# Kernel tuning notes

Hardware: AMD Instinct MI355X
Metric: run time of the kernel (lower is better)

The kernel has to match this reference:

```python
import jax, jax.numpy as jnp
import numpy as np

B, S, D, H = 2, 2048, 768, 12
DK = D // H
NEG = -1000000000.0


def setup_inputs() -> dict:
    key = jax.random.key(0)
    ks = jax.random.split(key, 12)
    inp = {
        "query": jax.random.normal(ks[0], (B, S, D), jnp.float32),
        "key": jax.random.normal(ks[1], (B, S, D), jnp.float32),
        "value": jax.random.normal(ks[2], (B, S, D), jnp.float32),
        "mask": jax.random.randint(ks[3], (B, 1, 1, S), 0, 2, jnp.int32),
    }
    sc = 1.0 / np.sqrt(D)
    inp["Wq"] = jax.random.normal(ks[4], (D, D), jnp.float32) * sc
    inp["bq"] = jnp.zeros((D,), jnp.float32)
    inp["Wk"] = jax.random.normal(ks[5], (D, D), jnp.float32) * sc
    inp["bk"] = jnp.zeros((D,), jnp.float32)
    inp["Wv"] = jax.random.normal(ks[6], (D, D), jnp.float32) * sc
    inp["bv"] = jnp.zeros((D,), jnp.float32)
    inp["Wo"] = jax.random.normal(ks[7], (D, D), jnp.float32) * sc
    inp["bo"] = jnp.zeros((D,), jnp.float32)
    return inp


def reference(query, key, value, mask, Wq, bq, Wk, bk, Wv, bv, Wo, bo):
    b = query.shape[0]
    # QKV projections -> [B, H, S, DK]
    def proj(x, W, bias):
        y = jnp.einsum('bsd,de->bse', x, W.T) + bias
        return y.reshape(b, -1, H, DK).transpose(0, 2, 1, 3)
    q = proj(query, Wq, bq)
    k = proj(key, Wk, bk)
    v = proj(value, Wv, bv)
    # scores: [B, H, S, S]
    scores = jnp.einsum('bhqd,bhkd->bhqk', q, k) / jnp.sqrt(jnp.float32(DK))
    scores = jnp.where(mask == 0, jnp.float32(NEG), scores)
    p = jax.nn.softmax(scores, axis=-1)
    x = jnp.einsum('bhqk,bhkd->bhqd', p, v)  # [B, H, S, DK]
    x = x.transpose(0, 2, 1, 3).reshape(b, -1, H * DK)
    return jnp.einsum('bsd,de->bse', x, Wo.T) + bo
```

## Files before the change

### kernel.cpp

```cpp
#include <hip/hip_runtime.h>

typedef unsigned short u16;
typedef __attribute__((ext_vector_type(8))) __bf16 bf16x8;
typedef __attribute__((ext_vector_type(8))) short s16x8;
typedef __attribute__((ext_vector_type(8))) unsigned short u16x8;
typedef __attribute__((ext_vector_type(4))) float f32x4;
typedef __attribute__((ext_vector_type(4))) unsigned short u16x4;
typedef __attribute__((ext_vector_type(4))) float fl4;
typedef __attribute__((ext_vector_type(4))) int i32x4;

#define MFMA(a, b, c) __builtin_amdgcn_mfma_f32_16x16x32_bf16((a), (b), (c), 0, 0, 0)
#define QSC 0.18033688011112042f

__device__ __forceinline__ u16 f2bf(float f) {
  __bf16 h = (__bf16)f;
  return __builtin_bit_cast(unsigned short, h);
}

__device__ __forceinline__ float bf2f(u16 u) {
  union { unsigned u; float f; } v; v.u = ((unsigned)u) << 16;
  return v.f;
}

__device__ __forceinline__ void gll16(const u16* g, u16* l) {
  typedef __attribute__((address_space(1))) unsigned int gu32;
  typedef __attribute__((address_space(3))) unsigned int lu32;
  __builtin_amdgcn_global_load_lds((gu32*)g, (lu32*)l, 16, 0, 0);
}


__global__ __launch_bounds__(256) void k_convert_w(
    const float* __restrict__ Wq, const float* __restrict__ Wk,
    const float* __restrict__ Wv, const float* __restrict__ Wo,
    u16* __restrict__ wqkv, u16* __restrict__ wob) {
  const int n = 3072 * 192;
  for (int i = blockIdx.x * 256 + threadIdx.x; i < n; i += gridDim.x * 256) {
    int row = i / 192;
    int col = (i - row * 192) * 4;
    const float* src; u16* dst; float sc = 1.0f;
    if (row < 768)       { src = Wq + row * 768;          dst = wqkv + row * 768; sc = QSC; }
    else if (row < 1536) { src = Wk + (row - 768) * 768;  dst = wqkv + row * 768; }
    else if (row < 2304) { src = Wv + (row - 1536) * 768; dst = wqkv + row * 768; }
    else                 { src = Wo + (row - 2304) * 768; dst = wob + (row - 2304) * 768; }
    fl4 f = *(const fl4*)(src + col);
    u16x4 o;
    o[0] = f2bf(f[0] * sc); o[1] = f2bf(f[1] * sc);
    o[2] = f2bf(f[2] * sc); o[3] = f2bf(f[3] * sc);
    *(u16x4*)(dst + col) = o;
  }
}


__global__ __launch_bounds__(256) void k_gemm_qkv(
    const float* __restrict__ xq, const float* __restrict__ xk,
    const float* __restrict__ xv, const u16* __restrict__ wqkv,
    const float* __restrict__ bq, const float* __restrict__ bk_,
    const float* __restrict__ bv_,
    u16* __restrict__ Qb, u16* __restrict__ Kb, u16* __restrict__ Vtb) {
  __shared__ __align__(16) u16 Abuf[2][128 * 32];
  __shared__ __align__(16) u16 Bbuf[2][128 * 32];
  const int tid = threadIdx.x;
  const int row0 = blockIdx.x * 128, col0 = blockIdx.y * 128;
  const int seg = col0 / 768;
  const float* A32 = (seg == 0) ? xq : ((seg == 1) ? xk : xv);
  const int w = tid >> 6, lane = tid & 63, lr = lane & 15, kg = lane >> 4;
  const int wr = (w >> 1) * 64, wc = (w & 1) * 64;

  const int c0 = tid, c1 = tid + 256;
  const int r0c = c0 >> 2, g0 = (c0 & 3) ^ ((r0c >> 1) & 3);
  const int r1c = c1 >> 2, g1 = (c1 & 3) ^ ((r1c >> 1) & 3);
  const float* aS0 = A32 + (size_t)(row0 + r0c) * 768 + g0 * 8;
  const float* aS1 = A32 + (size_t)(row0 + r1c) * 768 + g1 * 8;
  const u16* bS0 = wqkv + (size_t)(col0 + r0c) * 768 + g0 * 8;
  const u16* bS1 = wqkv + (size_t)(col0 + r1c) * 768 + g1 * 8;

  f32x4 acc[4][4];
  f32x4 zero = {0.f, 0.f, 0.f, 0.f};
#pragma unroll
  for (int i = 0; i < 4; i++)
#pragma unroll
    for (int j = 0; j < 4; j++) acc[i][j] = zero;

  int aoff[4], boff[4];
#pragma unroll
  for (int mi = 0; mi < 4; mi++) {
    int r = wr + mi * 16 + lr;
    aoff[mi] = r * 32 + (kg ^ ((r >> 1) & 3)) * 8;
  }
#pragma unroll
  for (int ni = 0; ni < 4; ni++) {
    int r = wc + ni * 16 + lr;
    boff[ni] = r * 32 + (kg ^ ((r >> 1) & 3)) * 8;
  }

  fl4 ar[4];
#define LOADA(kt) { ar[0] = *(const fl4*)(aS0 + (kt) * 32);       \
                    ar[1] = *(const fl4*)(aS0 + (kt) * 32 + 4);   \
                    ar[2] = *(const fl4*)(aS1 + (kt) * 32);       \
                    ar[3] = *(const fl4*)(aS1 + (kt) * 32 + 4); }
#define WRITEA(buf) { u16x8 t0, t1;                               \
    t0[0]=f2bf(ar[0][0]); t0[1]=f2bf(ar[0][1]); t0[2]=f2bf(ar[0][2]); t0[3]=f2bf(ar[0][3]); \
    t0[4]=f2bf(ar[1][0]); t0[5]=f2bf(ar[1][1]); t0[6]=f2bf(ar[1][2]); t0[7]=f2bf(ar[1][3]); \
    t1[0]=f2bf(ar[2][0]); t1[1]=f2bf(ar[2][1]); t1[2]=f2bf(ar[2][2]); t1[3]=f2bf(ar[2][3]); \
    t1[4]=f2bf(ar[3][0]); t1[5]=f2bf(ar[3][1]); t1[6]=f2bf(ar[3][2]); t1[7]=f2bf(ar[3][3]); \
    *(u16x8*)((buf) + c0 * 8) = t0; *(u16x8*)((buf) + c1 * 8) = t1; }
#define STAGEB(kt, buf) { gll16(bS0 + (kt) * 32, (buf) + c0 * 8); \
                          gll16(bS1 + (kt) * 32, (buf) + c1 * 8); }

  LOADA(0);
  STAGEB(0, Bbuf[0]);
  WRITEA(Abuf[0]);
  __syncthreads();

  for (int kt = 0; kt < 24; kt++) {
    const int cur = kt & 1;
    if (kt < 23) { LOADA(kt + 1); STAGEB(kt + 1, Bbuf[cur ^ 1]); }
    bf16x8 af[4], bfr[4];
#pragma unroll
    for (int mi = 0; mi < 4; mi++) af[mi] = *(const bf16x8*)(Abuf[cur] + aoff[mi]);
#pragma unroll
    for (int ni = 0; ni < 4; ni++) bfr[ni] = *(const bf16x8*)(Bbuf[cur] + boff[ni]);
#pragma unroll
    for (int mi = 0; mi < 4; mi++)
#pragma unroll
      for (int ni = 0; ni < 4; ni++)
        acc[mi][ni] = MFMA(af[mi], bfr[ni], acc[mi][ni]);
    __syncthreads();
    if (kt < 23) {
      WRITEA(Abuf[cur ^ 1]);
      __syncthreads();
    }
  }
#undef LOADA
#undef WRITEA
#undef STAGEB

  const float* bias = (seg == 0) ? bq : ((seg == 1) ? bk_ : bv_);
  const float bsc = (seg == 0) ? QSC : 1.0f;
  const int ncol0 = col0 - seg * 768;
#pragma unroll
  for (int ni = 0; ni < 4; ni++) {
    const int n = ncol0 + wc + ni * 16 + lr;
    const float bval = bias[n] * bsc;
    const int hh = n >> 6, dk = n & 63;
#pragma unroll
    for (int mi = 0; mi < 4; mi++)
#pragma unroll
      for (int j = 0; j < 4; j++) {
        const int m = row0 + wr + mi * 16 + kg * 4 + j;
        const int bb = m >> 11, ss = m & 2047;
        const u16 val = f2bf(acc[mi][ni][j] + bval);
        if (seg == 0)
          Qb[((size_t)((bb * 12 + hh) * 2048 + ss)) * 64 + dk] = val;
        else if (seg == 1)
          Kb[((size_t)((bb * 12 + hh) * 2048 + ss)) * 64 + dk] = val;
        else
          Vtb[((size_t)((bb * 12 + hh) * 64 + dk)) * 2048 + ss] = val;
      }
  }
}


__global__ __launch_bounds__(256) void k_attn(
    const u16* __restrict__ Qb, const u16* __restrict__ Kb,
    const u16* __restrict__ Vtb, const int* __restrict__ mask,
    u16* __restrict__ o_part, float* __restrict__ l_part) {
  __shared__ __align__(16) u16 Ks[2][64 * 64];
  __shared__ __align__(16) u16 Vs[2][64 * 64];
  __shared__ __align__(16) u16 Ps[4][32 * 64];
  __shared__ __align__(16) int mlds[1024];
  const int bid = blockIdx.x;
  const int wid = (bid & 7) * 96 + (bid >> 3);
  const int qt = wid & 15;
  const int gh = wid >> 4;
  const int bh = gh >> 1, half = gh & 1;
  const int b = bh / 12;
  const int kvb = half << 10;
  const int tid = threadIdx.x, w = tid >> 6, lane = tid & 63;
  const int lr = lane & 15, g = lane >> 4;
  const int q0 = qt * 128 + w * 32;
  const u16* Qh = Qb + (size_t)bh * (2048 * 64);
  const u16* Kh = Kb + (size_t)bh * (2048 * 64);
  const u16* Vh = Vtb + (size_t)bh * (64 * 2048);
  const int* mb = mask + b * 2048;
  u16* Pw = Ps[w];

  *(i32x4*)(mlds + tid * 4) = *(const i32x4*)(mb + kvb + tid * 4);

  bf16x8 aq[2][2];
#pragma unroll
  for (int mi = 0; mi < 2; mi++)
#pragma unroll
    for (int ks = 0; ks < 2; ks++)
      aq[mi][ks] = *(const bf16x8*)(Qh + (q0 + mi * 16 + lr) * 64 + ks * 32 + g * 8);

  f32x4 zero = {0.f, 0.f, 0.f, 0.f};
  f32x4 o[2][4];
#pragma unroll
  for (int mi = 0; mi < 2; mi++)
#pragma unroll
    for (int di = 0; di < 4; di++) o[mi][di] = zero;
  f32x4 o_l[2];
  o_l[0] = zero; o_l[1] = zero;

  s16x8 ov = {0x3F80, 0x3F80, 0x3F80, 0x3F80, 0x3F80, 0x3F80, 0x3F80, 0x3F80};
  bf16x8 ones = __builtin_bit_cast(bf16x8, ov);

  const int c0 = tid, c1 = tid + 256;
  const int sr0 = c0 >> 3, sg0 = (c0 & 7) ^ (sr0 & 7);
  const int sr1 = c1 >> 3, sg1 = (c1 & 7) ^ (sr1 & 7);
  const u16* kA0 = Kh + (size_t)kvb * 64 + sr0 * 64 + sg0 * 8;
  const u16* kA1 = Kh + (size_t)kvb * 64 + sr1 * 64 + sg1 * 8;
  const u16* vA0 = Vh + sr0 * 2048 + kvb + sg0 * 8;
  const u16* vA1 = Vh + sr1 * 2048 + kvb + sg1 * 8;

#define STAGE(u) { u16* kd = Ks[(u)&1]; u16* vd = Vs[(u)&1];           \
    gll16(kA0 + (u) * 4096, kd + c0 * 8);                              \
    gll16(kA1 + (u) * 4096, kd + c1 * 8);                              \
    gll16(vA0 + (u) * 64,  vd + c0 * 8);                               \
    gll16(vA1 + (u) * 64,  vd + c1 * 8); }

  STAGE(0);
  __syncthreads();

  for (int t = 0; t < 16; t++) {
    if (t < 15) STAGE(t + 1);
    const u16* Kc = Ks[t & 1];
    const u16* Vc = Vs[t & 1];

    f32x4 s[2][4];
#pragma unroll
    for (int ni = 0; ni < 4; ni++) {
      const int row = ni * 16 + lr;
      bf16x8 b0 = *(const bf16x8*)(Kc + row * 64 + ((g ^ (row & 7)) << 3));
      bf16x8 b1 = *(const bf16x8*)(Kc + row * 64 + (((4 + g) ^ (row & 7)) << 3));
#pragma unroll
      for (int mi = 0; mi < 2; mi++) {
        f32x4 z = zero;
        z = MFMA(aq[mi][0], b0, z);
        z = MFMA(aq[mi][1], b1, z);
        s[mi][ni] = z;
      }
    }
    int mk[4];
#pragma unroll
    for (int ni = 0; ni < 4; ni++) mk[ni] = mlds[t * 64 + ni * 16 + lr];
#pragma unroll
    for (int mi = 0; mi < 2; mi++)
#pragma unroll
      for (int ni = 0; ni < 4; ni++)
#pragma unroll
        for (int j = 0; j < 4; j++)
          s[mi][ni][j] = mk[ni] ? s[mi][ni][j] : -1e9f;

#pragma unroll
    for (int mi = 0; mi < 2; mi++)
#pragma unroll
      for (int ni = 0; ni < 4; ni++)
#pragma unroll
        for (int j = 0; j < 4; j++) {
          const float p = __builtin_amdgcn_exp2f(s[mi][ni][j]);
          const int prow = mi * 16 + g * 4 + j;
          const int byt = prow * 128 + ((ni * 32 + lr * 2) ^ ((prow & 7) << 4));
          Pw[byt >> 1] = f2bf(p);
        }

#pragma unroll
    for (int ks2 = 0; ks2 < 2; ks2++) {
      bf16x8 ap[2];
#pragma unroll
      for (int mi = 0; mi < 2; mi++) {
        const int prow = mi * 16 + lr;
        const int byt = prow * 128 + ((ks2 * 64 + g * 16) ^ ((prow & 7) << 4));
        ap[mi] = *(const bf16x8*)(Pw + (byt >> 1));
      }
#pragma unroll
      for (int di = 0; di < 4; di++) {
        const int vrow = di * 16 + lr;
        bf16x8 bv = *(const bf16x8*)(Vc + vrow * 64 + (((ks2 * 4 + g) ^ (vrow & 7)) << 3));
#pragma unroll
        for (int mi = 0; mi < 2; mi++)
          o[mi][di] = MFMA(ap[mi], bv, o[mi][di]);
      }
#pragma unroll
      for (int mi = 0; mi < 2; mi++)
        o_l[mi] = MFMA(ap[mi], ones, o_l[mi]);
    }

    if (t < 15) __syncthreads();
  }
#undef STAGE

  u16* opw = o_part + (size_t)(half * 24 + bh) * (2048 * 64);
  float* lpw = l_part + (size_t)(half * 24 + bh) * 2048;
#pragma unroll
  for (int mi = 0; mi < 2; mi++) {
#pragma unroll
    for (int di = 0; di < 4; di++)
#pragma unroll
      for (int j = 0; j < 4; j++) {
        const int row = q0 + mi * 16 + g * 4 + j;
        opw[(size_t)row * 64 + di * 16 + lr] = f2bf(o[mi][di][j]);
      }
    if (lr == 0) {
#pragma unroll
      for (int j = 0; j < 4; j++)
        lpw[q0 + mi * 16 + g * 4 + j] = o_l[mi][j];
    }
  }
}


__global__ __launch_bounds__(256) void k_combine(
    const u16* __restrict__ o_part, const float* __restrict__ l_part,
    u16* __restrict__ attn) {
  const int idx = blockIdx.x * 256 + threadIdx.x;
  const int row = idx >> 3;
  const int c8 = (idx & 7) << 3;
  const size_t HALF_O = (size_t)24 * 2048 * 64;
  u16x8 a0 = *(const u16x8*)(o_part + (size_t)row * 64 + c8);
  u16x8 a1 = *(const u16x8*)(o_part + HALF_O + (size_t)row * 64 + c8);
  const float l = l_part[row] + l_part[24 * 2048 + row];
  const float rcp = 1.0f / l;
  u16x8 r;
#pragma unroll
  for (int j = 0; j < 8; j++)
    r[j] = f2bf((bf2f(a0[j]) + bf2f(a1[j])) * rcp);
  const int bh = row >> 11, s = row & 2047;
  const int b = bh / 12, h = bh - b * 12;
  *(u16x8*)(attn + (size_t)(b * 2048 + s) * 768 + h * 64 + c8) = r;
}


__global__ __launch_bounds__(256) void k_gemm_out(
    const u16* __restrict__ attn, const u16* __restrict__ wob,
    const float* __restrict__ bo, float* __restrict__ out) {
  __shared__ __align__(16) u16 As[2][128 * 32];
  __shared__ __align__(16) u16 Bs[2][128 * 32];
  const int tid = threadIdx.x;
  const int row0 = blockIdx.x * 128, col0 = blockIdx.y * 128;
  const int w = tid >> 6, lane = tid & 63, lr = lane & 15, kg = lane >> 4;
  const int wr = (w >> 1) * 64, wc = (w & 1) * 64;

  const int c0 = tid, c1 = tid + 256;
  const int r0c = c0 >> 2, g0 = (c0 & 3) ^ ((r0c >> 1) & 3);
  const int r1c = c1 >> 2, g1 = (c1 & 3) ^ ((r1c >> 1) & 3);
  const u16* aS0 = attn + (size_t)(row0 + r0c) * 768 + g0 * 8;
  const u16* aS1 = attn + (size_t)(row0 + r1c) * 768 + g1 * 8;
  const u16* bS0 = wob + (size_t)(col0 + r0c) * 768 + g0 * 8;
  const u16* bS1 = wob + (size_t)(col0 + r1c) * 768 + g1 * 8;

  f32x4 acc[4][4];
  f32x4 zero = {0.f, 0.f, 0.f, 0.f};
#pragma unroll
  for (int i = 0; i < 4; i++)
#pragma unroll
    for (int j = 0; j < 4; j++) acc[i][j] = zero;

  int aoff[4], boff[4];
#pragma unroll
  for (int mi = 0; mi < 4; mi++) {
    int r = wr + mi * 16 + lr;
    aoff[mi] = r * 32 + (kg ^ ((r >> 1) & 3)) * 8;
  }
#pragma unroll
  for (int ni = 0; ni < 4; ni++) {
    int r = wc + ni * 16 + lr;
    boff[ni] = r * 32 + (kg ^ ((r >> 1) & 3)) * 8;
  }

#define STAGE(kt) { u16* ad = As[(kt)&1]; u16* bd = Bs[(kt)&1];   \
    gll16(aS0 + (kt) * 32, ad + c0 * 8);                          \
    gll16(aS1 + (kt) * 32, ad + c1 * 8);                          \
    gll16(bS0 + (kt) * 32, bd + c0 * 8);                          \
    gll16(bS1 + (kt) * 32, bd + c1 * 8); }

  STAGE(0);
  __syncthreads();

  for (int kt = 0; kt < 24; kt++) {
    const int cur = kt & 1;
    if (kt < 23) STAGE(kt + 1);
    bf16x8 af[4], bfr[4];
#pragma unroll
    for (int mi = 0; mi < 4; mi++) af[mi] = *(const bf16x8*)(As[cur] + aoff[mi]);
#pragma unroll
    for (int ni = 0; ni < 4; ni++) bfr[ni] = *(const bf16x8*)(Bs[cur] + boff[ni]);
#pragma unroll
    for (int mi = 0; mi < 4; mi++)
#pragma unroll
      for (int ni = 0; ni < 4; ni++)
        acc[mi][ni] = MFMA(af[mi], bfr[ni], acc[mi][ni]);
    if (kt < 23) __syncthreads();
  }
#undef STAGE

#pragma unroll
  for (int ni = 0; ni < 4; ni++) {
    const int n = col0 + wc + ni * 16 + lr;
    const float bval = bo[n];
#pragma unroll
    for (int mi = 0; mi < 4; mi++)
#pragma unroll
      for (int j = 0; j < 4; j++) {
        const int m = row0 + wr + mi * 16 + kg * 4 + j;
        out[(size_t)m * 768 + n] = acc[mi][ni][j] + bval;
      }
  }
}


extern "C" void kernel_launch(void* const* d_in, const int* in_sizes, int n_in,
                              void* d_out, int out_size, void* d_ws, size_t ws_size,
                              hipStream_t stream) {
  const float* q = (const float*)d_in[0];
  const float* k = (const float*)d_in[1];
  const float* v = (const float*)d_in[2];
  const int* mask = (const int*)d_in[3];
  const float* Wq = (const float*)d_in[4];
  const float* bq = (const float*)d_in[5];
  const float* Wk = (const float*)d_in[6];
  const float* bk = (const float*)d_in[7];
  const float* Wv = (const float*)d_in[8];
  const float* bv = (const float*)d_in[9];
  const float* Wo = (const float*)d_in[10];
  const float* bo = (const float*)d_in[11];
  float* out = (float*)d_out;

  u16* scratch = (u16*)d_ws;
  u16* wqkv = scratch + (size_t)3 * 4096 * 768;
  u16* wob = wqkv + (size_t)2304 * 768;
  u16* Qb = wob + (size_t)768 * 768;
  u16* Kb = Qb + (size_t)4096 * 768;
  u16* Vtb = Kb + (size_t)4096 * 768;
  u16* attn = Vtb + (size_t)4096 * 768;

  u16* o_part = scratch;
  float* l_part = (float*)(scratch + (size_t)2 * 24 * 2048 * 64);

  k_convert_w<<<dim3(2304), dim3(256), 0, stream>>>(Wq, Wk, Wv, Wo, wqkv, wob);
  k_gemm_qkv<<<dim3(32, 18), dim3(256), 0, stream>>>(q, k, v, wqkv, bq, bk, bv, Qb, Kb, Vtb);
  k_attn<<<dim3(768), dim3(256), 0, stream>>>(Qb, Kb, Vtb, mask, o_part, l_part);
  k_combine<<<dim3(1536), dim3(256), 0, stream>>>(o_part, l_part, attn);
  k_gemm_out<<<dim3(32, 6), dim3(256), 0, stream>>>(attn, wob, bo, out);
}
```

Measured before the change: 122.1 us.

## Swap MFMA operands for transposed scores and remap GEMM blocks across XCDs

In the attention kernel the QK^T MFMA operands are swapped, so each lane holds four consecutive key columns of one query row. The mask can then be read as a single int4 vector load, and P is written to LDS as packed 4-element bf16 stores instead of scalar 2-byte writes. Separately, both projection GEMMs now run on a 1D grid whose block index is remapped so that consecutive tiles land on the same XCD (bid&7 striding), aiming to improve L2 reuse. The risk is that the P layout and swizzle must still match the later PV reads.

```diff
diff --git a/kernel.cpp b/kernel.cpp
--- a/kernel.cpp
+++ b/kernel.cpp
@@ -60,7 +60,9 @@
   __shared__ __align__(16) u16 Abuf[2][128 * 32];
   __shared__ __align__(16) u16 Bbuf[2][128 * 32];
   const int tid = threadIdx.x;
-  const int row0 = blockIdx.x * 128, col0 = blockIdx.y * 128;
+  const int bid = blockIdx.x;
+  const int wid = (bid & 7) * 72 + (bid >> 3);
+  const int row0 = (wid / 18) * 128, col0 = (wid % 18) * 128;
   const int seg = col0 / 768;
   const float* A32 = (seg == 0) ? xq : ((seg == 1) ? xk : xv);
   const int w = tid >> 6, lane = tid & 63, lr = lane & 15, kg = lane >> 4;
@@ -236,34 +238,34 @@
       bf16x8 b1 = *(const bf16x8*)(Kc + row * 64 + (((4 + g) ^ (row & 7)) << 3));
 #pragma unroll
       for (int mi = 0; mi < 2; mi++) {
-        f32x4 z = zero;
-        z = MFMA(aq[mi][0], b0, z);
-        z = MFMA(aq[mi][1], b1, z);
+        f32x4 z = MFMA(b0, aq[mi][0], zero);
+        z = MFMA(b1, aq[mi][1], z);
         s[mi][ni] = z;
       }
     }
-    int mk[4];
-#pragma unroll
-    for (int ni = 0; ni < 4; ni++) mk[ni] = mlds[t * 64 + ni * 16 + lr];
-#pragma unroll
-    for (int mi = 0; mi < 2; mi++)
-#pragma unroll
-      for (int ni = 0; ni < 4; ni++)
+#pragma unroll
+    for (int ni = 0; ni < 4; ni++) {
+      const i32x4 mk4 = *(const i32x4*)(mlds + t * 64 + ni * 16 + g * 4);
+#pragma unroll
+      for (int mi = 0; mi < 2; mi++)
 #pragma unroll
         for (int j = 0; j < 4; j++)
-          s[mi][ni][j] = mk[ni] ? s[mi][ni][j] : -1e9f;
-
-#pragma unroll
-    for (int mi = 0; mi < 2; mi++)
-#pragma unroll
-      for (int ni = 0; ni < 4; ni++)
-#pragma unroll
-        for (int j = 0; j < 4; j++) {
-          const float p = __builtin_amdgcn_exp2f(s[mi][ni][j]);
-          const int prow = mi * 16 + g * 4 + j;
-          const int byt = prow * 128 + ((ni * 32 + lr * 2) ^ ((prow & 7) << 4));
-          Pw[byt >> 1] = f2bf(p);
-        }
+          s[mi][ni][j] = mk4[j] ? s[mi][ni][j] : -1e9f;
+    }
+
+#pragma unroll
+    for (int mi = 0; mi < 2; mi++) {
+      const int prow = mi * 16 + lr;
+      const int rbase = prow * 128, sw = (prow & 7) << 4;
+#pragma unroll
+      for (int ni = 0; ni < 4; ni++) {
+        u16x4 pk;
+#pragma unroll
+        for (int j = 0; j < 4; j++)
+          pk[j] = f2bf(__builtin_amdgcn_exp2f(s[mi][ni][j]));
+        *(u16x4*)(Pw + ((rbase + ((ni * 32 + g * 8) ^ sw)) >> 1)) = pk;
+      }
+    }
 
 #pragma unroll
     for (int ks2 = 0; ks2 < 2; ks2++) {
@@ -338,7 +340,9 @@
   __shared__ __align__(16) u16 As[2][128 * 32];
   __shared__ __align__(16) u16 Bs[2][128 * 32];
   const int tid = threadIdx.x;
-  const int row0 = blockIdx.x * 128, col0 = blockIdx.y * 128;
+  const int bid = blockIdx.x;
+  const int wid = (bid & 7) * 24 + (bid >> 3);
+  const int row0 = (wid / 6) * 128, col0 = (wid % 6) * 128;
   const int w = tid >> 6, lane = tid & 63, lr = lane & 15, kg = lane >> 4;
   const int wr = (w >> 1) * 64, wc = (w & 1) * 64;
 
@@ -439,8 +443,8 @@
   float* l_part = (float*)(scratch + (size_t)2 * 24 * 2048 * 64);
 
   k_convert_w<<<dim3(2304), dim3(256), 0, stream>>>(Wq, Wk, Wv, Wo, wqkv, wob);
-  k_gemm_qkv<<<dim3(32, 18), dim3(256), 0, stream>>>(q, k, v, wqkv, bq, bk, bv, Qb, Kb, Vtb);
+  k_gemm_qkv<<<dim3(576), dim3(256), 0, stream>>>(q, k, v, wqkv, bq, bk, bv, Qb, Kb, Vtb);
   k_attn<<<dim3(768), dim3(256), 0, stream>>>(Qb, Kb, Vtb, mask, o_part, l_part);
   k_combine<<<dim3(1536), dim3(256), 0, stream>>>(o_part, l_part, attn);
-  k_gemm_out<<<dim3(32, 6), dim3(256), 0, stream>>>(attn, wob, bo, out);
-}
+  k_gemm_out<<<dim3(192), dim3(256), 0, stream>>>(attn, wob, bo, out);
+}
```

Measured after the change: 112.6 us. 1.08x faster.
